# Performance work log

Measured on AMD Instinct MI355X. Metric: run time of the kernel, lower is better.

## Reference

```python
import jax, jax.numpy as jnp
import numpy as np

N = 4096

def setup_inputs() -> dict:
    key = jax.random.key(0)
    kA, kB = jax.random.split(key)
    A = jnp.tril(jax.random.normal(kA, (N, N), dtype=jnp.float32))
    B = jnp.tril(jax.random.normal(kB, (N, N), dtype=jnp.float32))
    return {"A": A, "B": B}

def reference(A, B):
    # Product of two lower-triangular matrices; result is lower-triangular.
    # tril applied to the dense matmul reproduces the intended math exactly
    # (and zeroes any numerical noise in the structural-zero upper triangle).
    return jnp.tril(jnp.matmul(A, B))
```

## Files before the change

### kernel.cpp

```cpp
#include <hip/hip_runtime.h>
#include <stdint.h>

#define NN 4096
#define NB 32
#define BK 32

#define NHUNITS 272
#define ZBASE 664
#define TGRID 1160

#define PGRID 8328

typedef __bf16 bf16x8 __attribute__((ext_vector_type(8)));
typedef float f32x4 __attribute__((ext_vector_type(4)));
typedef unsigned short ushort8 __attribute__((ext_vector_type(8)));

__device__ __forceinline__ unsigned short f2bf(float x) {
    union { float f; unsigned int u; } v; v.f = x;
    unsigned int u = v.u;
    u += 0x7fffu + ((u >> 16) & 1u);
    return (unsigned short)(u >> 16);
}

#define GLOAD16(g, l) __builtin_amdgcn_global_load_lds( \
    (const __attribute__((address_space(1))) unsigned int*)(g), \
    (__attribute__((address_space(3))) unsigned int*)(l), 16, 0, 0)

__device__ __forceinline__ void heavy_map(int h, int& bi, int& bj) {
    int t = h, d = NB - 1;
    while (t >= NB - d) { t -= NB - d; --d; }
    bj = t; bi = t + d;
}

__global__ __launch_bounds__(256) void prep(const float* __restrict__ A,
                                            const float* __restrict__ B,
                                            unsigned short* __restrict__ Ab,
                                            unsigned short* __restrict__ Bt,
                                            float* __restrict__ C) {
    __shared__ float tile[64][65];
    int bid = blockIdx.x;
    int tid = threadIdx.x;

    if (bid < 4096) {
        int i = bid;
        int nslots = (((i >> 7) + 1) * 128) >> 3;
        const float4* src = reinterpret_cast<const float4*>(A + (size_t)i * NN);
        unsigned short* dst = Ab + (size_t)i * NN;
        for (int p = tid; p < nslots; p += 256) {
            float4 x0 = src[p * 2], x1 = src[p * 2 + 1];
            ushort8 o;
            o[0] = f2bf(x0.x); o[1] = f2bf(x0.y); o[2] = f2bf(x0.z); o[3] = f2bf(x0.w);
            o[4] = f2bf(x1.x); o[5] = f2bf(x1.y); o[6] = f2bf(x1.z); o[7] = f2bf(x1.w);
            *reinterpret_cast<ushort8*>(dst + p * 8) = o;
        }
        return;
    }
    if (bid < 8192) {
        int s = bid - 4096;
        int n64 = s >> 6, k64 = s & 63;
        if (k64 < (n64 & ~1)) return;
        int n0 = n64 * 64, k0 = k64 * 64;
        int tx = tid & 63, ty = tid >> 6;
#pragma unroll
        for (int r = 0; r < 16; ++r) {
            int k = ty + r * 4;
            tile[k][tx] = B[(size_t)(k0 + k) * NN + n0 + tx];
        }
        __syncthreads();
#pragma unroll
        for (int r = 0; r < 16; ++r) {
            int n = ty + r * 4;
            Bt[(size_t)(n0 + n) * NN + k0 + tx] = f2bf(tile[tx][n]);
        }
        return;
    }
    int h = bid - 8192;
    int bi, bj; heavy_map(h, bi, bj);
    float4 z = make_float4(0.f, 0.f, 0.f, 0.f);
    float4* cp = reinterpret_cast<float4*>(C + (size_t)bi * 128 * NN + (size_t)bj * 128);
#pragma unroll
    for (int i2 = 0; i2 < 16; ++i2) {
        int slot = tid + i2 * 256;
        int row = slot >> 5, c4 = slot & 31;
        cp[(size_t)row * (NN / 4) + c4] = z;
    }
}

__global__ __launch_bounds__(256) void trimm(const unsigned short* __restrict__ Ab,
                                             const unsigned short* __restrict__ Bt,
                                             float* __restrict__ C) {
    int bid = blockIdx.x;
    int tid = threadIdx.x;
    int lane = tid & 63;
    int w = tid >> 6;

    int bi, bj;
    bool heavy = false;
    int k_lo, k_hi;

    if (bid >= ZBASE) {
        int t = bid - ZBASE;
        int r = 0, cnt = NB - 1;
        while (t >= cnt) { t -= cnt; ++r; --cnt; }
        bi = r; bj = r + 1 + t;
        float4 z = make_float4(0.f, 0.f, 0.f, 0.f);
        float4* cp = reinterpret_cast<float4*>(C + (size_t)bi * 128 * NN + (size_t)bj * 128);
#pragma unroll
        for (int i2 = 0; i2 < 16; ++i2) {
            int slot = tid + i2 * 256;
            int row = slot >> 5, c4 = slot & 31;
            cp[(size_t)row * (NN / 4) + c4] = z;
        }
        return;
    }
    if (bid < NHUNITS) {
        heavy = true;
        int h = bid >> 1, half = bid & 1;
        heavy_map(h, bi, bj);
        k_lo = bj * 128;
        k_hi = (bi + 1) * 128;
        int len = (k_hi - k_lo) >> 1;
        if (half == 0) k_hi = k_lo + len;
        else           k_lo = k_lo + len;
    } else {
        int t = bid - NHUNITS, d = 15;
        while (t >= NB - d) { t -= NB - d; --d; }
        bj = t; bi = t + d;
        k_lo = bj * 128;
        k_hi = (bi + 1) * 128;
    }

    __shared__ unsigned short As[2][128 * BK];
    __shared__ unsigned short Bs[2][128 * BK];

    int wr = w >> 1, wc = w & 1;

    int srow = w * 32 + (lane >> 2);
    int skoff = (((lane & 3) ^ ((lane >> 3) & 3)) * 8);
    const unsigned short* gA0 = Ab + (size_t)(bi * 128 + srow) * NN + skoff;
    const unsigned short* gA1 = gA0 + (size_t)16 * NN;
    const unsigned short* gB0 = Bt + (size_t)(bj * 128 + srow) * NN + skoff;
    const unsigned short* gB1 = gB0 + (size_t)16 * NN;

    f32x4 acc[4][4];
#pragma unroll
    for (int mi = 0; mi < 4; ++mi)
#pragma unroll
        for (int ni = 0; ni < 4; ++ni)
            acc[mi][ni] = (f32x4){0.f, 0.f, 0.f, 0.f};

    int arow = wr * 64 + (lane & 15);
    int brow = wc * 64 + (lane & 15);
    int kq = (((lane >> 4) ^ ((lane >> 1) & 3)) * 8);

#define STAGE(bufsel, kk) do { \
        unsigned short* a_ = &As[bufsel][w * 1024]; \
        unsigned short* b_ = &Bs[bufsel][w * 1024]; \
        GLOAD16(gA0 + (kk), a_); \
        GLOAD16(gA1 + (kk), a_ + 512); \
        GLOAD16(gB0 + (kk), b_); \
        GLOAD16(gB1 + (kk), b_ + 512); \
    } while (0)

    STAGE(0, k_lo);
    {
        int k1 = (k_lo + BK < k_hi) ? (k_lo + BK) : k_lo;
        STAGE(1, k1);
    }
    int cur = 0;

    for (int kt = k_lo; kt < k_hi; kt += BK) {
        asm volatile("s_waitcnt vmcnt(4)" ::: "memory");
        __builtin_amdgcn_s_barrier();

        bf16x8 af[4], bfr[4];
#pragma unroll
        for (int mi = 0; mi < 4; ++mi)
            af[mi] = *reinterpret_cast<const bf16x8*>(&As[cur][(arow + mi * 16) * BK + kq]);
#pragma unroll
        for (int ni = 0; ni < 4; ++ni)
            bfr[ni] = *reinterpret_cast<const bf16x8*>(&Bs[cur][(brow + ni * 16) * BK + kq]);
#pragma unroll
        for (int mi = 0; mi < 4; ++mi)
#pragma unroll
            for (int ni = 0; ni < 4; ++ni)
                acc[mi][ni] = __builtin_amdgcn_mfma_f32_16x16x32_bf16(af[mi], bfr[ni], acc[mi][ni], 0, 0, 0);

        __builtin_amdgcn_s_barrier();

        int kn = kt + 2 * BK;
        if (kn >= k_hi) kn = k_lo;
        STAGE(cur, kn);

        cur ^= 1;
    }
    asm volatile("s_waitcnt vmcnt(0)" ::: "memory");
#undef STAGE

    int crow0 = bi * 128 + wr * 64 + (lane >> 4) * 4;
    int ccol0 = bj * 128 + wc * 64 + (lane & 15);
    if (heavy) {
#pragma unroll
        for (int mi = 0; mi < 4; ++mi)
#pragma unroll
            for (int ni = 0; ni < 4; ++ni) {
                float* cp = C + (size_t)(crow0 + mi * 16) * NN + ccol0 + ni * 16;
#pragma unroll
                for (int r2 = 0; r2 < 4; ++r2)
                    atomicAdd(&cp[(size_t)r2 * NN], acc[mi][ni][r2]);
            }
    } else {
#pragma unroll
        for (int mi = 0; mi < 4; ++mi)
#pragma unroll
            for (int ni = 0; ni < 4; ++ni) {
                float* cp = C + (size_t)(crow0 + mi * 16) * NN + ccol0 + ni * 16;
#pragma unroll
                for (int r2 = 0; r2 < 4; ++r2)
                    cp[(size_t)r2 * NN] = acc[mi][ni][r2];
            }
    }
}

extern "C" void kernel_launch(void* const* d_in, const int* in_sizes, int n_in,
                              void* d_out, int out_size, void* d_ws, size_t ws_size,
                              hipStream_t stream) {
    const float* A = (const float*)d_in[0];
    const float* B = (const float*)d_in[1];
    float* C = (float*)d_out;
    unsigned short* Ab = (unsigned short*)d_ws;
    unsigned short* Bt = Ab + (size_t)NN * NN;
    prep<<<PGRID, 256, 0, stream>>>(A, B, Ab, Bt, C);
    trimm<<<TGRID, 256, 0, stream>>>(Ab, Bt, C);
}
```

Before: 88.68 us.

## Enlarge triangular GEMM tiles to 256x256 with 8 waves and phased MFMA schedule

Moves from 128x128 tiles with BK=32 and 4 waves to 256x256 tiles with BK=64 and 8 waves (512 threads). Each wave computes a 128x64 subtile in four barrier-separated MFMA phases, with s_setprio raised around the MFMA blocks and XOR-swizzled LDS. The larger tiles cut redundant global and LDS traffic per FLOP. The cost is fewer blocks (292 versus 1160) on a 256-CU part, coarser triangular granularity that does wasted work on the diagonal, and higher LDS and register pressure (128KB LDS per block).

```diff
diff --git a/kernel.cpp b/kernel.cpp
--- a/kernel.cpp
+++ b/kernel.cpp
@@ -2,14 +2,14 @@
 #include <stdint.h>
 
 #define NN 4096
-#define NB 32
-#define BK 32
-
-#define NHUNITS 272
-#define ZBASE 664
-#define TGRID 1160
-
-#define PGRID 8328
+#define NB2 16
+#define BK2 64
+
+#define NHUNITS 72
+#define NUNITS 172
+#define TGRID 292
+
+#define PGRID 8336
 
 typedef __bf16 bf16x8 __attribute__((ext_vector_type(8)));
 typedef float f32x4 __attribute__((ext_vector_type(4)));
@@ -26,10 +26,10 @@
     (const __attribute__((address_space(1))) unsigned int*)(g), \
     (__attribute__((address_space(3))) unsigned int*)(l), 16, 0, 0)
 
-__device__ __forceinline__ void heavy_map(int h, int& bi, int& bj) {
-    int t = h, d = NB - 1;
-    while (t >= NB - d) { t -= NB - d; --d; }
-    bj = t; bi = t + d;
+__device__ __forceinline__ void split_map(int z, int& bi, int& bj) {
+    int d = 15;
+    while (z >= NB2 - d) { z -= NB2 - d; --d; }
+    bj = z; bi = z + d;
 }
 
 __global__ __launch_bounds__(256) void prep(const float* __restrict__ A,
@@ -43,7 +43,7 @@
 
     if (bid < 4096) {
         int i = bid;
-        int nslots = (((i >> 7) + 1) * 128) >> 3;
+        int nslots = ((i >> 8) + 1) * 32;
         const float4* src = reinterpret_cast<const float4*>(A + (size_t)i * NN);
         unsigned short* dst = Ab + (size_t)i * NN;
         for (int p = tid; p < nslots; p += 256) {
@@ -58,7 +58,7 @@
     if (bid < 8192) {
         int s = bid - 4096;
         int n64 = s >> 6, k64 = s & 63;
-        if (k64 < (n64 & ~1)) return;
+        if (k64 < (n64 & ~3)) return;
         int n0 = n64 * 64, k0 = k64 * 64;
         int tx = tid & 63, ty = tid >> 6;
 #pragma unroll
@@ -74,150 +74,191 @@
         }
         return;
     }
-    int h = bid - 8192;
-    int bi, bj; heavy_map(h, bi, bj);
-    float4 z = make_float4(0.f, 0.f, 0.f, 0.f);
-    float4* cp = reinterpret_cast<float4*>(C + (size_t)bi * 128 * NN + (size_t)bj * 128);
-#pragma unroll
-    for (int i2 = 0; i2 < 16; ++i2) {
-        int slot = tid + i2 * 256;
-        int row = slot >> 5, c4 = slot & 31;
-        cp[(size_t)row * (NN / 4) + c4] = z;
-    }
-}
-
-__global__ __launch_bounds__(256) void trimm(const unsigned short* __restrict__ Ab,
-                                             const unsigned short* __restrict__ Bt,
-                                             float* __restrict__ C) {
+    {
+        int zb = bid - 8192;
+        int bi, bj; split_map(zb >> 2, bi, bj);
+        int part = zb & 3;
+        float4 zf = make_float4(0.f, 0.f, 0.f, 0.f);
+        float4* cp = reinterpret_cast<float4*>(C + (size_t)(bi * 256 + part * 64) * NN + (size_t)bj * 256);
+#pragma unroll
+        for (int i2 = 0; i2 < 16; ++i2) {
+            int slot = tid + i2 * 256;
+            int row = slot >> 6, c4 = slot & 63;
+            cp[(size_t)row * (NN / 4) + c4] = zf;
+        }
+    }
+}
+
+__global__ __launch_bounds__(512, 2) void trimm(const unsigned short* __restrict__ Ab,
+                                                const unsigned short* __restrict__ Bt,
+                                                float* __restrict__ C) {
     int bid = blockIdx.x;
     int tid = threadIdx.x;
     int lane = tid & 63;
     int w = tid >> 6;
 
-    int bi, bj;
-    bool heavy = false;
-    int k_lo, k_hi;
-
-    if (bid >= ZBASE) {
-        int t = bid - ZBASE;
-        int r = 0, cnt = NB - 1;
-        while (t >= cnt) { t -= cnt; ++r; --cnt; }
-        bi = r; bj = r + 1 + t;
+    if (bid >= NUNITS) {
+        int r = bid - NUNITS, bi = 0;
+        while (r >= NB2 - 1 - bi) { r -= NB2 - 1 - bi; ++bi; }
+        int bj = bi + 1 + r;
         float4 z = make_float4(0.f, 0.f, 0.f, 0.f);
-        float4* cp = reinterpret_cast<float4*>(C + (size_t)bi * 128 * NN + (size_t)bj * 128);
-#pragma unroll
-        for (int i2 = 0; i2 < 16; ++i2) {
-            int slot = tid + i2 * 256;
-            int row = slot >> 5, c4 = slot & 31;
+        float4* cp = reinterpret_cast<float4*>(C + (size_t)bi * 256 * NN + (size_t)bj * 256);
+#pragma unroll
+        for (int i2 = 0; i2 < 32; ++i2) {
+            int slot = tid + i2 * 512;
+            int row = slot >> 6, c4 = slot & 63;
             cp[(size_t)row * (NN / 4) + c4] = z;
         }
         return;
     }
+
+    int bi, bj, k_lo, k_hi;
+    bool atom;
     if (bid < NHUNITS) {
-        heavy = true;
-        int h = bid >> 1, half = bid & 1;
-        heavy_map(h, bi, bj);
-        k_lo = bj * 128;
-        k_hi = (bi + 1) * 128;
-        int len = (k_hi - k_lo) >> 1;
-        if (half == 0) k_hi = k_lo + len;
-        else           k_lo = k_lo + len;
+        atom = true;
+        int r = bid, d = 15;
+        while (r >= 2 * (NB2 - d)) { r -= 2 * (NB2 - d); --d; }
+        int t = r >> 1, half = r & 1;
+        bj = t; bi = t + d;
+        int base = bj * 256, len = (d + 1) * 128;
+        k_lo = base + (half ? len : 0);
+        k_hi = k_lo + len;
     } else {
-        int t = bid - NHUNITS, d = 15;
-        while (t >= NB - d) { t -= NB - d; --d; }
-        bj = t; bi = t + d;
-        k_lo = bj * 128;
-        k_hi = (bi + 1) * 128;
-    }
-
-    __shared__ unsigned short As[2][128 * BK];
-    __shared__ unsigned short Bs[2][128 * BK];
-
-    int wr = w >> 1, wc = w & 1;
-
-    int srow = w * 32 + (lane >> 2);
-    int skoff = (((lane & 3) ^ ((lane >> 3) & 3)) * 8);
-    const unsigned short* gA0 = Ab + (size_t)(bi * 128 + srow) * NN + skoff;
-    const unsigned short* gA1 = gA0 + (size_t)16 * NN;
-    const unsigned short* gB0 = Bt + (size_t)(bj * 128 + srow) * NN + skoff;
-    const unsigned short* gB1 = gB0 + (size_t)16 * NN;
-
-    f32x4 acc[4][4];
-#pragma unroll
-    for (int mi = 0; mi < 4; ++mi)
-#pragma unroll
-        for (int ni = 0; ni < 4; ++ni)
-            acc[mi][ni] = (f32x4){0.f, 0.f, 0.f, 0.f};
-
-    int arow = wr * 64 + (lane & 15);
-    int brow = wc * 64 + (lane & 15);
-    int kq = (((lane >> 4) ^ ((lane >> 1) & 3)) * 8);
+        atom = false;
+        int r = bid - NHUNITS, d = 7;
+        while (r >= NB2 - d) { r -= NB2 - d; --d; }
+        bj = r; bi = r + d;
+        k_lo = bj * 256;
+        k_hi = (bi + 1) * 256;
+    }
+
+    __shared__ unsigned short As[2][256 * 64];
+    __shared__ unsigned short Bs[2][256 * 64];
+
+    int wr = w >> 2;
+    int wc = w & 3;
+
+    int srow = tid >> 3;
+    int sgch = (tid & 7) ^ (srow & 7);
+    const unsigned short* gAs = Ab + (size_t)(bi * 256 + srow) * NN + sgch * 8;
+    const unsigned short* gBs = Bt + (size_t)(bj * 256 + srow) * NN + sgch * 8;
+
+    int fr = lane & 15;
+    int ch0 = ((lane >> 4)) ^ (lane & 7);
+    int ch1 = (4 | (lane >> 4)) ^ (lane & 7);
+
+    f32x4 acc[8][4];
+#pragma unroll
+    for (int m = 0; m < 8; ++m)
+#pragma unroll
+        for (int n = 0; n < 4; ++n)
+            acc[m][n] = (f32x4){0.f, 0.f, 0.f, 0.f};
+
+    bf16x8 Aq[8], B0q[4], B1q[4];
 
 #define STAGE(bufsel, kk) do { \
-        unsigned short* a_ = &As[bufsel][w * 1024]; \
-        unsigned short* b_ = &Bs[bufsel][w * 1024]; \
-        GLOAD16(gA0 + (kk), a_); \
-        GLOAD16(gA1 + (kk), a_ + 512); \
-        GLOAD16(gB0 + (kk), b_); \
-        GLOAD16(gB1 + (kk), b_ + 512); \
-    } while (0)
+        unsigned short* la_ = &As[bufsel][0] + tid * 8; \
+        unsigned short* lb_ = &Bs[bufsel][0] + tid * 8; \
+        GLOAD16(gAs + (kk), la_); \
+        GLOAD16(gAs + (kk) + 64 * NN, la_ + 4096); \
+        GLOAD16(gAs + (kk) + 128 * NN, la_ + 8192); \
+        GLOAD16(gAs + (kk) + 192 * NN, la_ + 12288); \
+        GLOAD16(gBs + (kk), lb_); \
+        GLOAD16(gBs + (kk) + 64 * NN, lb_ + 4096); \
+        GLOAD16(gBs + (kk) + 128 * NN, lb_ + 8192); \
+        GLOAD16(gBs + (kk) + 192 * NN, lb_ + 12288); \
+    } while (0)
+
+#define LDA(MH) do { \
+        _Pragma("unroll") for (int m_ = 0; m_ < 4; ++m_) { \
+            int row_ = wr * 128 + ((MH) * 4 + m_) * 16 + fr; \
+            Aq[m_ * 2 + 0] = *reinterpret_cast<const bf16x8*>(&Ac[row_ * 64 + ch0 * 8]); \
+            Aq[m_ * 2 + 1] = *reinterpret_cast<const bf16x8*>(&Ac[row_ * 64 + ch1 * 8]); \
+        } \
+    } while (0)
+
+#define LDB(NH, BQ) do { \
+        _Pragma("unroll") for (int n_ = 0; n_ < 2; ++n_) { \
+            int row_ = wc * 64 + ((NH) * 2 + n_) * 16 + fr; \
+            BQ[n_ * 2 + 0] = *reinterpret_cast<const bf16x8*>(&Bc[row_ * 64 + ch0 * 8]); \
+            BQ[n_ * 2 + 1] = *reinterpret_cast<const bf16x8*>(&Bc[row_ * 64 + ch1 * 8]); \
+        } \
+    } while (0)
+
+#define MFMA16(MB, NBASE, BQ) do { \
+        _Pragma("unroll") for (int m_ = 0; m_ < 4; ++m_) \
+        _Pragma("unroll") for (int n_ = 0; n_ < 2; ++n_) { \
+            acc[(MB) + m_][(NBASE) + n_] = __builtin_amdgcn_mfma_f32_16x16x32_bf16( \
+                Aq[m_ * 2 + 0], BQ[n_ * 2 + 0], acc[(MB) + m_][(NBASE) + n_], 0, 0, 0); \
+            acc[(MB) + m_][(NBASE) + n_] = __builtin_amdgcn_mfma_f32_16x16x32_bf16( \
+                Aq[m_ * 2 + 1], BQ[n_ * 2 + 1], acc[(MB) + m_][(NBASE) + n_], 0, 0, 0); \
+        } \
+    } while (0)
+
+    int nt = (k_hi - k_lo) >> 6;
 
     STAGE(0, k_lo);
-    {
-        int k1 = (k_lo + BK < k_hi) ? (k_lo + BK) : k_lo;
-        STAGE(1, k1);
-    }
-    int cur = 0;
-
-    for (int kt = k_lo; kt < k_hi; kt += BK) {
-        asm volatile("s_waitcnt vmcnt(4)" ::: "memory");
-        __builtin_amdgcn_s_barrier();
-
-        bf16x8 af[4], bfr[4];
-#pragma unroll
-        for (int mi = 0; mi < 4; ++mi)
-            af[mi] = *reinterpret_cast<const bf16x8*>(&As[cur][(arow + mi * 16) * BK + kq]);
-#pragma unroll
-        for (int ni = 0; ni < 4; ++ni)
-            bfr[ni] = *reinterpret_cast<const bf16x8*>(&Bs[cur][(brow + ni * 16) * BK + kq]);
-#pragma unroll
-        for (int mi = 0; mi < 4; ++mi)
-#pragma unroll
-            for (int ni = 0; ni < 4; ++ni)
-                acc[mi][ni] = __builtin_amdgcn_mfma_f32_16x16x32_bf16(af[mi], bfr[ni], acc[mi][ni], 0, 0, 0);
-
-        __builtin_amdgcn_s_barrier();
-
-        int kn = kt + 2 * BK;
-        if (kn >= k_hi) kn = k_lo;
-        STAGE(cur, kn);
-
-        cur ^= 1;
-    }
-    asm volatile("s_waitcnt vmcnt(0)" ::: "memory");
+    __syncthreads();
+
+    for (int t = 0; t < nt; ++t) {
+        int cur = t & 1;
+        const unsigned short* Ac = &As[cur][0];
+        const unsigned short* Bc = &Bs[cur][0];
+
+        LDA(0);
+        LDB(0, B0q);
+        if (t + 1 < nt) STAGE(cur ^ 1, k_lo + (t + 1) * BK2);
+        __builtin_amdgcn_s_barrier();
+        __builtin_amdgcn_s_setprio(1);
+        MFMA16(0, 0, B0q);
+        __builtin_amdgcn_s_setprio(0);
+        __builtin_amdgcn_s_barrier();
+
+        LDB(1, B1q);
+        __builtin_amdgcn_s_barrier();
+        __builtin_amdgcn_s_setprio(1);
+        MFMA16(0, 2, B1q);
+        __builtin_amdgcn_s_setprio(0);
+        __builtin_amdgcn_s_barrier();
+
+        LDA(1);
+        __builtin_amdgcn_s_barrier();
+        __builtin_amdgcn_s_setprio(1);
+        MFMA16(4, 2, B1q);
+        __builtin_amdgcn_s_setprio(0);
+        __builtin_amdgcn_s_barrier();
+
+        __builtin_amdgcn_s_setprio(1);
+        MFMA16(4, 0, B0q);
+        __builtin_amdgcn_s_setprio(0);
+        __syncthreads();
+    }
 #undef STAGE
-
-    int crow0 = bi * 128 + wr * 64 + (lane >> 4) * 4;
-    int ccol0 = bj * 128 + wc * 64 + (lane & 15);
-    if (heavy) {
-#pragma unroll
-        for (int mi = 0; mi < 4; ++mi)
-#pragma unroll
-            for (int ni = 0; ni < 4; ++ni) {
-                float* cp = C + (size_t)(crow0 + mi * 16) * NN + ccol0 + ni * 16;
+#undef LDA
+#undef LDB
+#undef MFMA16
+
+    int crow0 = bi * 256 + wr * 128 + (lane >> 4) * 4;
+    int ccol0 = bj * 256 + wc * 64 + fr;
+    if (atom) {
+#pragma unroll
+        for (int m = 0; m < 8; ++m)
+#pragma unroll
+            for (int n = 0; n < 4; ++n) {
+                float* cp = C + (size_t)(crow0 + m * 16) * NN + ccol0 + n * 16;
 #pragma unroll
                 for (int r2 = 0; r2 < 4; ++r2)
-                    atomicAdd(&cp[(size_t)r2 * NN], acc[mi][ni][r2]);
+                    atomicAdd(&cp[(size_t)r2 * NN], acc[m][n][r2]);
             }
     } else {
 #pragma unroll
-        for (int mi = 0; mi < 4; ++mi)
-#pragma unroll
-            for (int ni = 0; ni < 4; ++ni) {
-                float* cp = C + (size_t)(crow0 + mi * 16) * NN + ccol0 + ni * 16;
+        for (int m = 0; m < 8; ++m)
+#pragma unroll
+            for (int n = 0; n < 4; ++n) {
+                float* cp = C + (size_t)(crow0 + m * 16) * NN + ccol0 + n * 16;
 #pragma unroll
                 for (int r2 = 0; r2 < 4; ++r2)
-                    cp[(size_t)r2 * NN] = acc[mi][ni][r2];
+                    cp[(size_t)r2 * NN] = acc[m][n][r2];
             }
     }
 }
@@ -231,5 +272,5 @@
     unsigned short* Ab = (unsigned short*)d_ws;
     unsigned short* Bt = Ab + (size_t)NN * NN;
     prep<<<PGRID, 256, 0, stream>>>(A, B, Ab, Bt, C);
-    trimm<<<TGRID, 256, 0, stream>>>(Ab, Bt, C);
-}
+    trimm<<<TGRID, 512, 0, stream>>>(Ab, Bt, C);
+}
```

Measured after the change: 86.21 us. 1.03x faster.

## Double the K tile to 64 with a new swizzled LDS staging layout

Applied to the files above, without the earlier changes.

Raises the per-iteration K depth from 32 to 64, so each barrier pair covers two MFMA steps per output tile and each thread issues eight async global-to-LDS loads per stage. The LDS layout changes to a whole-block row mapping with an XOR swizzle over 8 chunks to avoid bank conflicts, and launch bounds now request two blocks per CU. This aims to halve the barrier and loop overhead per unit of work. LDS use doubles to 64KB per block, which may limit occupancy, and k ranges must be multiples of 64 for the new trip count to be correct.

```diff
diff --git a/kernel.cpp b/kernel.cpp
--- a/kernel.cpp
+++ b/kernel.cpp
@@ -3,7 +3,7 @@
 
 #define NN 4096
 #define NB 32
-#define BK 32
+#define BK 64
 
 #define NHUNITS 272
 #define ZBASE 664
@@ -86,9 +86,9 @@
     }
 }
 
-__global__ __launch_bounds__(256) void trimm(const unsigned short* __restrict__ Ab,
-                                             const unsigned short* __restrict__ Bt,
-                                             float* __restrict__ C) {
+__global__ __launch_bounds__(256, 2) void trimm(const unsigned short* __restrict__ Ab,
+                                                const unsigned short* __restrict__ Bt,
+                                                float* __restrict__ C) {
     int bid = blockIdx.x;
     int tid = threadIdx.x;
     int lane = tid & 63;
@@ -135,12 +135,10 @@
 
     int wr = w >> 1, wc = w & 1;
 
-    int srow = w * 32 + (lane >> 2);
-    int skoff = (((lane & 3) ^ ((lane >> 3) & 3)) * 8);
-    const unsigned short* gA0 = Ab + (size_t)(bi * 128 + srow) * NN + skoff;
-    const unsigned short* gA1 = gA0 + (size_t)16 * NN;
-    const unsigned short* gB0 = Bt + (size_t)(bj * 128 + srow) * NN + skoff;
-    const unsigned short* gB1 = gB0 + (size_t)16 * NN;
+    int srow = tid >> 3;
+    int schunk = ((tid & 7) ^ (srow & 7)) * 8;
+    const unsigned short* gA = Ab + (size_t)(bi * 128 + srow) * NN + schunk;
+    const unsigned short* gB = Bt + (size_t)(bj * 128 + srow) * NN + schunk;
 
     f32x4 acc[4][4];
 #pragma unroll
@@ -149,46 +147,59 @@
         for (int ni = 0; ni < 4; ++ni)
             acc[mi][ni] = (f32x4){0.f, 0.f, 0.f, 0.f};
 
-    int arow = wr * 64 + (lane & 15);
-    int brow = wc * 64 + (lane & 15);
-    int kq = (((lane >> 4) ^ ((lane >> 1) & 3)) * 8);
+    int fr = lane & 15;
+    int c0 = (((lane >> 4) ^ (lane & 7)) * 8);
+    int c1 = ((((lane >> 4) | 4) ^ (lane & 7)) * 8);
+    int arow = wr * 64 + fr;
+    int brow = wc * 64 + fr;
 
 #define STAGE(bufsel, kk) do { \
-        unsigned short* a_ = &As[bufsel][w * 1024]; \
-        unsigned short* b_ = &Bs[bufsel][w * 1024]; \
-        GLOAD16(gA0 + (kk), a_); \
-        GLOAD16(gA1 + (kk), a_ + 512); \
-        GLOAD16(gB0 + (kk), b_); \
-        GLOAD16(gB1 + (kk), b_ + 512); \
+        unsigned short* la_ = &As[bufsel][0] + tid * 8; \
+        unsigned short* lb_ = &Bs[bufsel][0] + tid * 8; \
+        GLOAD16(gA + (kk), la_); \
+        GLOAD16(gA + (kk) + (size_t)32 * NN, la_ + 2048); \
+        GLOAD16(gA + (kk) + (size_t)64 * NN, la_ + 4096); \
+        GLOAD16(gA + (kk) + (size_t)96 * NN, la_ + 6144); \
+        GLOAD16(gB + (kk), lb_); \
+        GLOAD16(gB + (kk) + (size_t)32 * NN, lb_ + 2048); \
+        GLOAD16(gB + (kk) + (size_t)64 * NN, lb_ + 4096); \
+        GLOAD16(gB + (kk) + (size_t)96 * NN, lb_ + 6144); \
     } while (0)
 
+    int nt = (k_hi - k_lo) >> 6;
+
     STAGE(0, k_lo);
-    {
-        int k1 = (k_lo + BK < k_hi) ? (k_lo + BK) : k_lo;
-        STAGE(1, k1);
-    }
+    STAGE(1, k_lo + BK);
     int cur = 0;
 
-    for (int kt = k_lo; kt < k_hi; kt += BK) {
-        asm volatile("s_waitcnt vmcnt(4)" ::: "memory");
+    for (int t = 0; t < nt; ++t) {
+        asm volatile("s_waitcnt vmcnt(8)" ::: "memory");
         __builtin_amdgcn_s_barrier();
 
-        bf16x8 af[4], bfr[4];
-#pragma unroll
-        for (int mi = 0; mi < 4; ++mi)
-            af[mi] = *reinterpret_cast<const bf16x8*>(&As[cur][(arow + mi * 16) * BK + kq]);
-#pragma unroll
-        for (int ni = 0; ni < 4; ++ni)
-            bfr[ni] = *reinterpret_cast<const bf16x8*>(&Bs[cur][(brow + ni * 16) * BK + kq]);
-#pragma unroll
-        for (int mi = 0; mi < 4; ++mi)
-#pragma unroll
-            for (int ni = 0; ni < 4; ++ni)
-                acc[mi][ni] = __builtin_amdgcn_mfma_f32_16x16x32_bf16(af[mi], bfr[ni], acc[mi][ni], 0, 0, 0);
+        const unsigned short* Ac = &As[cur][0];
+        const unsigned short* Bc = &Bs[cur][0];
+        bf16x8 a0[4], a1[4], b0[4], b1[4];
+#pragma unroll
+        for (int m = 0; m < 4; ++m) {
+            a0[m] = *reinterpret_cast<const bf16x8*>(&Ac[(arow + m * 16) * BK + c0]);
+            a1[m] = *reinterpret_cast<const bf16x8*>(&Ac[(arow + m * 16) * BK + c1]);
+        }
+#pragma unroll
+        for (int n = 0; n < 4; ++n) {
+            b0[n] = *reinterpret_cast<const bf16x8*>(&Bc[(brow + n * 16) * BK + c0]);
+            b1[n] = *reinterpret_cast<const bf16x8*>(&Bc[(brow + n * 16) * BK + c1]);
+        }
+#pragma unroll
+        for (int m = 0; m < 4; ++m)
+#pragma unroll
+            for (int n = 0; n < 4; ++n) {
+                acc[m][n] = __builtin_amdgcn_mfma_f32_16x16x32_bf16(a0[m], b0[n], acc[m][n], 0, 0, 0);
+                acc[m][n] = __builtin_amdgcn_mfma_f32_16x16x32_bf16(a1[m], b1[n], acc[m][n], 0, 0, 0);
+            }
 
         __builtin_amdgcn_s_barrier();
 
-        int kn = kt + 2 * BK;
+        int kn = k_lo + (t + 2) * BK;
         if (kn >= k_hi) kn = k_lo;
         STAGE(cur, kn);
 
@@ -198,7 +209,7 @@
 #undef STAGE
 
     int crow0 = bi * 128 + wr * 64 + (lane >> 4) * 4;
-    int ccol0 = bj * 128 + wc * 64 + (lane & 15);
+    int ccol0 = bj * 128 + wc * 64 + fr;
     if (heavy) {
 #pragma unroll
         for (int mi = 0; mi < 4; ++mi)
```

Measured after the change: 75.68 us. 14.7% less time.
